# Kernel tuning notes

Measured on AMD Instinct MI355X. Metric: run time of the kernel, lower is better.

## Reference

```python
import jax, jax.numpy as jnp
import numpy as np
from jax import lax

EPS = 1e-5
HEADS = 4
NPOINT = 512


def _layernorm(x, g, b):
    mu = jnp.mean(x, axis=-1, keepdims=True)
    var = jnp.var(x, axis=-1, keepdims=True)
    return (x - mu) * lax.rsqrt(var + EPS) * g + b


def farthest_point_sample(xyz, npoint):
    # xyz: [B, N, 3] -> idx [B, npoint]  (canonical PointNet++ FPS, seeded at point 0)
    B, N, _ = xyz.shape

    def step(carry, _):
        dist, far = carry  # [B,N], [B]
        centroid = jnp.take_along_axis(xyz, far[:, None, None], axis=1)  # [B,1,3]
        d = jnp.sum((xyz - centroid) ** 2, axis=-1)  # [B,N]
        dist = jnp.minimum(dist, d)
        nxt = jnp.argmax(dist, axis=1).astype(jnp.int32)
        return (dist, nxt), far

    init = (jnp.full((B, N), 1e10, xyz.dtype), jnp.zeros((B,), jnp.int32))
    _, idx = lax.scan(step, init, None, length=npoint)  # [npoint, B]
    return idx.T  # [B, npoint]


def index_points(points, idx):
    # points: [B, N, D], idx: [B, S] -> [B, S, D]
    return jnp.take_along_axis(points, idx[..., None], axis=1)


def setup_inputs() -> dict:
    key = jax.random.key(0)
    ks = iter(jax.random.split(key, 16))
    B, N, Cin, D, Dff, Dout = 8, 2048, 64, 128, 512, 256
    w = lambda k, s: (jax.random.normal(k, s, jnp.float32) * 0.02)
    inp = {
        "xyz": jax.random.normal(next(ks), (B, 3, N), jnp.float32),
        "points": jax.random.normal(next(ks), (B, Cin, N), jnp.float32),
        "W_proj": w(next(ks), (D, Cin)), "b_proj": jnp.zeros((D,)),
        "bn1_g": jnp.ones((D,)), "bn1_b": jnp.zeros((D,)),
        "bn1_m": jnp.zeros((D,)), "bn1_v": jnp.ones((D,)),
        "W_pos": w(next(ks), (D, 3)), "b_pos": jnp.zeros((D,)),
        "Wq": w(next(ks), (D, D)), "bq": jnp.zeros((D,)),
        "Wk": w(next(ks), (D, D)), "bk": jnp.zeros((D,)),
        "Wv": w(next(ks), (D, D)), "bv": jnp.zeros((D,)),
        "Wo": w(next(ks), (D, D)), "bo": jnp.zeros((D,)),
        "ln1_g": jnp.ones((D,)), "ln1_b": jnp.zeros((D,)),
        "W1": w(next(ks), (Dff, D)), "b1": jnp.zeros((Dff,)),
        "W2": w(next(ks), (D, Dff)), "b2": jnp.zeros((D,)),
        "ln2_g": jnp.ones((D,)), "ln2_b": jnp.zeros((D,)),
        "W_fc": w(next(ks), (Dout, D + 3)), "b_fc": jnp.zeros((Dout,)),
        "bn2_g": jnp.ones((Dout,)), "bn2_b": jnp.zeros((Dout,)),
        "bn2_m": jnp.zeros((Dout,)), "bn2_v": jnp.ones((Dout,)),
    }
    return inp


def reference(xyz, points, W_proj, b_proj, bn1_g, bn1_b, bn1_m, bn1_v,
              W_pos, b_pos, Wq, bq, Wk, bk, Wv, bv, Wo, bo,
              ln1_g, ln1_b, W1, b1, W2, b2, ln2_g, ln2_b,
              W_fc, b_fc, bn2_g, bn2_b, bn2_m, bn2_v):
    B, _, N = xyz.shape
    D = W_proj.shape[0]
    hd = D // HEADS

    # project: pointwise conv + BN (inference), output [B, N, D]
    feat = jnp.einsum('dc,bcn->bnd', W_proj, points) + b_proj
    feat = (feat - bn1_m) * lax.rsqrt(bn1_v + EPS) * bn1_g + bn1_b

    # transformer block with xyz positional encoding
    pos = jnp.einsum('dc,bcn->bnd', W_pos, xyz) + b_pos
    x = feat + pos
    q = (x @ Wq.T + bq).reshape(B, N, HEADS, hd)
    k = (x @ Wk.T + bk).reshape(B, N, HEADS, hd)
    v = (x @ Wv.T + bv).reshape(B, N, HEADS, hd)
    scores = jnp.einsum('bnhd,bmhd->bhnm', q, k) / jnp.sqrt(jnp.float32(hd))
    attn = jax.nn.softmax(scores, axis=-1)
    o = jnp.einsum('bhnm,bmhd->bnhd', attn, v).reshape(B, N, D)
    x = _layernorm(x + (o @ Wo.T + bo), ln1_g, ln1_b)
    ffn = jax.nn.relu(x @ W1.T + b1) @ W2.T + b2
    features = _layernorm(x + ffn, ln2_g, ln2_b)  # [B, N, D]

    # sampling + gather
    xyz_t = jnp.transpose(xyz, (0, 2, 1))  # [B, N, 3]
    fps_idx = farthest_point_sample(xyz_t, NPOINT)  # [B, npoint]
    new_points = index_points(features, fps_idx)    # [B, npoint, D]
    new_xyz = index_points(xyz_t, fps_idx)          # [B, npoint, 3]

    cat = jnp.concatenate([new_points, new_xyz], axis=-1)  # [B, npoint, D+3]
    out = jnp.einsum('od,bnd->bon', W_fc, cat) + b_fc[None, :, None]
    out = (out - bn2_m[None, :, None]) * lax.rsqrt(bn2_v + EPS)[None, :, None] \
          * bn2_g[None, :, None] + bn2_b[None, :, None]
    out = jax.nn.relu(out)  # [B, Dout, npoint]

    return jnp.transpose(new_xyz, (0, 2, 1)), out
```

## Files before the change

### kernel.cpp

```cpp
#include <hip/hip_runtime.h>
#include <hip/hip_bf16.h>

#define B_    8
#define N_    2048
#define CIN_  64
#define D_    128
#define DFF_  512
#define DOUT_ 256
#define S_    512
#define H_    4
#define HD_   32
#define EPS_  1e-5f

typedef unsigned short u16;
typedef unsigned long long u64;
typedef __attribute__((ext_vector_type(8))) short short8v;
typedef __attribute__((ext_vector_type(4))) float f32x4;

__device__ __forceinline__ u16 f2bu(float f) {
  __hip_bfloat16 h = __float2bfloat16(f);
  return *(u16*)&h;
}
__device__ __forceinline__ float bu2f(u16 u) {
  __hip_bfloat16 h = *(__hip_bfloat16*)&u;
  return __bfloat162float(h);
}

#define OW_QKV 0
#define OW_O   49152
#define OW_1   65536
#define OW_2   131072
#define OW_FC  196608
#define OW_CAT 237568
#define NW_TOT 249856

__global__ __launch_bounds__(256) void prep_kernel(
    const float* __restrict__ Wq, const float* __restrict__ bq,
    const float* __restrict__ Wk, const float* __restrict__ bk,
    const float* __restrict__ Wv, const float* __restrict__ bv,
    const float* __restrict__ Wo, const float* __restrict__ W1,
    const float* __restrict__ W2, const float* __restrict__ Wfc,
    const float* __restrict__ bfc, const float* __restrict__ Wp,
    const float* __restrict__ bp, const float* __restrict__ Wpos,
    const float* __restrict__ bpos, const float* __restrict__ g1,
    const float* __restrict__ be1, const float* __restrict__ m1,
    const float* __restrict__ v1, const float* __restrict__ g2,
    const float* __restrict__ bb2, const float* __restrict__ m2,
    const float* __restrict__ v2, u16* __restrict__ wb,
    float* __restrict__ fb) {
  const float SC = 0.1767766952966369f;
  int i = blockIdx.x * 256 + threadIdx.x;
  if (i < OW_O) {
    int n = i >> 7, k = i & 127;
    float v = (n < 128) ? Wq[i] * SC
                        : (n < 256) ? Wk[(n - 128) * 128 + k]
                                    : Wv[(n - 256) * 128 + k];
    wb[OW_QKV + i] = f2bu(v);
  } else if (i < OW_1) {
    wb[i] = f2bu(Wo[i - OW_O]);
  } else if (i < OW_2) {
    wb[i] = f2bu(W1[i - OW_1]);
  } else if (i < OW_FC) {
    wb[i] = f2bu(W2[i - OW_2]);
  } else if (i < OW_CAT) {
    int j = i - OW_FC;
    int n = j / 160, c = j % 160;
    wb[i] = f2bu(c < 131 ? Wfc[n * 131 + c] : 0.f);
  } else if (i < NW_TOT) {
    int j = i - OW_CAT;
    int d = j / 96, c = j % 96;
    float v;
    if (c < 64) v = Wp[d * 64 + c] * (g1[d] * rsqrtf(v1[d] + EPS_));
    else if (c < 67) v = Wpos[d * 3 + (c - 64)];
    else v = 0.f;
    wb[i] = f2bu(v);
  } else if (i < NW_TOT + 384) {
    int n = i - NW_TOT;
    fb[n] = (n < 128) ? bq[n] * SC : (n < 256) ? bk[n - 128] : bv[n - 256];
  } else if (i < NW_TOT + 512) {
    int d = i - (NW_TOT + 384);
    float s1 = g1[d] * rsqrtf(v1[d] + EPS_);
    fb[384 + d] = (bp[d] - m1[d]) * s1 + be1[d] + bpos[d];
  } else if (i < NW_TOT + 768) {
    int n = i - (NW_TOT + 512);
    fb[512 + n] = g2[n] * rsqrtf(v2[n] + EPS_);
  } else if (i < NW_TOT + 1024) {
    int n = i - (NW_TOT + 768);
    float s = g2[n] * rsqrtf(v2[n] + EPS_);
    fb[768 + n] = bfc[n] * s + bb2[n] - m2[n] * s;
  }
}

#define FPS_SMEM 24704

template <int CTRL, int RM>
__device__ __forceinline__ float dppmax(float v) {
  int m = __builtin_amdgcn_update_dpp(__float_as_int(v), __float_as_int(v),
                                      CTRL, RM, 0xF, true);
  return fmaxf(v, __int_as_float(m));
}

__device__ __forceinline__ void fps_slice(
    char* smem, int b, const float* __restrict__ xyz,
    float* __restrict__ dist_ws, int* __restrict__ far_ws,
    int* __restrict__ idx_out, float* __restrict__ out0, int s0, int s1) {
  float* xs = (float*)smem;
  u64* keys = (u64*)(smem + 3 * N_ * 4);
  const int t = threadIdx.x, w = t >> 6, lane = t & 63;
  const float* xb = xyz + (size_t)b * 3 * N_;
  for (int i = t; i < 3 * N_; i += 256) xs[i] = xb[i];
  const int base = w * 512 + lane * 8;
  float* dw = dist_ws + b * N_;
  float dist[8];
  if (s0 == 0) {
#pragma unroll
    for (int j = 0; j < 8; j++) dist[j] = 1e10f;
  } else {
#pragma unroll
    for (int j = 0; j < 8; j++) dist[j] = dw[base + j];
  }
  int far = (s0 == 0) ? 0 : far_ws[b];
  __syncthreads();
  float px[8], py[8], pz[8];
#pragma unroll
  for (int j = 0; j < 8; j++) {
    px[j] = xs[base + j];
    py[j] = xs[N_ + base + j];
    pz[j] = xs[2 * N_ + base + j];
  }
  float cx = xs[far], cy = xs[N_ + far], cz = xs[2 * N_ + far];
  for (int s = s0; s < s1; s++) {
    if (t == 0) {
      idx_out[b * S_ + s] = far;
      out0[(size_t)b * 3 * S_ + s] = cx;
      out0[(size_t)b * 3 * S_ + S_ + s] = cy;
      out0[(size_t)b * 3 * S_ + 2 * S_ + s] = cz;
    }
    float best = -1.0f;
    int bestp = 0;
#pragma unroll
    for (int j = 0; j < 8; j++) {
      float dx = __fsub_rn(px[j], cx);
      float dy = __fsub_rn(py[j], cy);
      float dz = __fsub_rn(pz[j], cz);
      float d = __fadd_rn(__fadd_rn(__fmul_rn(dx, dx), __fmul_rn(dy, dy)),
                          __fmul_rn(dz, dz));
      float nd = fminf(dist[j], d);
      dist[j] = nd;
      if (nd > best) { best = nd; bestp = base + j; }
    }
    float m = best;
    m = dppmax<0x111, 0xF>(m);
    m = dppmax<0x112, 0xF>(m);
    m = dppmax<0x114, 0xF>(m);
    m = dppmax<0x118, 0xF>(m);
    m = dppmax<0x142, 0xA>(m);
    m = dppmax<0x143, 0xC>(m);
    float M = __int_as_float(__builtin_amdgcn_readlane(__float_as_int(m), 63));
    u64 mask = __ballot(best == M);
    int wl = __ffsll((long long)mask) - 1;
    int wp = __builtin_amdgcn_readlane(bestp, wl);
    if (lane == 0)
      keys[(s & 1) * 4 + w] = ((u64)__float_as_uint(M) << 32) |
                              (unsigned)(0xFFFFFFFFu - (unsigned)wp);
    __syncthreads();
    const u64* kp = keys + (s & 1) * 4;
    u64 k0 = kp[0], k1 = kp[1], k2 = kp[2], k3 = kp[3];
    u64 ka = k0 > k1 ? k0 : k1;
    u64 kb2 = k2 > k3 ? k2 : k3;
    u64 kk = ka > kb2 ? ka : kb2;
    far = (int)(0xFFFFFFFFu - (unsigned)kk);
    cx = xs[far];
    cy = xs[N_ + far];
    cz = xs[2 * N_ + far];
  }
#pragma unroll
  for (int j = 0; j < 8; j++) dw[base + j] = dist[j];
  if (t == 0) far_ws[b] = far;
}

template <int K, int KC, int ASTAGE, int EPI>
__global__ __launch_bounds__(256) void gemm_k(
    const u16* __restrict__ A, const u16* __restrict__ W,
    const float* __restrict__ srcf0, const float* __restrict__ srcf1,
    const int* __restrict__ fidx, const float* __restrict__ p0,
    const float* __restrict__ p1, const float* __restrict__ p2,
    const u16* __restrict__ resid, u16* __restrict__ outb,
    float* __restrict__ outf, int ntn, int fpsnb, int s0, int s1,
    const float* fxyz, float* fdist, int* ffar, int* fidxo, float* fout0) {
  constexpr int KP = KC + 8;
  constexpr int GEMM_SMEM = 2 * 128 * KP * 2;
  constexpr int SMEM = GEMM_SMEM > FPS_SMEM ? GEMM_SMEM : FPS_SMEM;
  __shared__ __align__(16) char smem[SMEM];
  if ((int)blockIdx.x < fpsnb) {
    fps_slice(smem, blockIdx.x, fxyz, fdist, ffar, fidxo, fout0, s0, s1);
    return;
  }
  u16 (*As)[KP] = (u16 (*)[KP])smem;
  u16 (*Ws)[KP] = (u16 (*)[KP])(smem + 128 * KP * 2);
  const int bid = blockIdx.x - fpsnb;
  const int mt = bid / ntn, nt = bid % ntn;
  const int t = threadIdx.x, w = t >> 6, lane = t & 63;
  const int g = lane >> 4, lr = lane & 15;

  f32x4 acc[2][8];
#pragma unroll
  for (int qf = 0; qf < 2; qf++)
#pragma unroll
    for (int nf = 0; nf < 8; nf++) acc[qf][nf] = {0.f, 0.f, 0.f, 0.f};

  for (int kc = 0; kc < K / KC; kc++) {
    __syncthreads();
    for (int i = t; i < 128 * (KC / 8); i += 256) {
      int row = i / (KC / 8), c8 = i % (KC / 8);
      *(short8v*)&Ws[row][c8 * 8] =
          *(const short8v*)(W + (size_t)(nt * 128 + row) * K + kc * KC + c8 * 8);
    }
    if constexpr (ASTAGE == 0) {
      for (int i = t; i < 128 * (KC / 8); i += 256) {
        int row = i / (KC / 8), c8 = i % (KC / 8);
        *(short8v*)&As[row][c8 * 8] =
            *(const short8v*)(A + (size_t)(mt * 128 + row) * K + kc * KC + c8 * 8);
      }
    } else if constexpr (ASTAGE == 1) {
      int bb = (mt * 128) >> 11, n0 = (mt * 128) & (N_ - 1);
      for (int i = t; i < 96 * 128; i += 256) {
        int c = i >> 7, n = i & 127;
        float v;
        if (c < 64) v = srcf0[((size_t)bb * CIN_ + c) * N_ + n0 + n];
        else if (c < 67) v = srcf1[((size_t)bb * 3 + (c - 64)) * N_ + n0 + n];
        else v = 0.f;
        As[n][c] = f2bu(v);
      }
    } else {
      int bb = (mt * 128) >> 9, sq0 = (mt * 128) & (S_ - 1);
      for (int i = t; i < 128 * 20; i += 256) {
        int row = i / 20, c8 = i % 20;
        int id = fidx[bb * S_ + sq0 + row];
        short8v val;
        if (c8 < 16) {
          val = *(const short8v*)(A + ((size_t)bb * N_ + id) * D_ + c8 * 8);
        } else if (c8 == 16) {
          val = short8v{0, 0, 0, 0, 0, 0, 0, 0};
          val[0] = (short)f2bu(srcf1[((size_t)bb * 3 + 0) * N_ + id]);
          val[1] = (short)f2bu(srcf1[((size_t)bb * 3 + 1) * N_ + id]);
          val[2] = (short)f2bu(srcf1[((size_t)bb * 3 + 2) * N_ + id]);
        } else {
          val = short8v{0, 0, 0, 0, 0, 0, 0, 0};
        }
        *(short8v*)&As[row][c8 * 8] = val;
      }
    }
    __syncthreads();
#pragma unroll
    for (int ks = 0; ks < KC / 32; ks++) {
      short8v a0 = *(const short8v*)&As[w * 32 + lr][ks * 32 + 8 * g];
      short8v a1 = *(const short8v*)&As[w * 32 + 16 + lr][ks * 32 + 8 * g];
#pragma unroll
      for (int nf = 0; nf < 8; nf++) {
        short8v bb = *(const short8v*)&Ws[nf * 16 + lr][ks * 32 + 8 * g];
        acc[0][nf] = __builtin_amdgcn_mfma_f32_16x16x32_bf16(a0, bb, acc[0][nf], 0, 0, 0);
        acc[1][nf] = __builtin_amdgcn_mfma_f32_16x16x32_bf16(a1, bb, acc[1][nf], 0, 0, 0);
      }
    }
  }

  if constexpr (EPI == 3) {
#pragma unroll
    for (int qf = 0; qf < 2; qf++) {
#pragma unroll
      for (int i = 0; i < 4; i++) {
        int m = mt * 128 + w * 32 + qf * 16 + 4 * g + i;
        float v[8], sm = 0.f, sq = 0.f;
#pragma unroll
        for (int nf = 0; nf < 8; nf++) {
          int n = nf * 16 + lr;
          float x = acc[qf][nf][i] + p0[n] + bu2f(resid[(size_t)m * D_ + n]);
          v[nf] = x;
          sm += x;
          sq += x * x;
        }
#pragma unroll
        for (int msk = 1; msk < 16; msk <<= 1) {
          sm += __shfl_xor(sm, msk);
          sq += __shfl_xor(sq, msk);
        }
        float mu = sm * (1.f / 128.f);
        float var = sq * (1.f / 128.f) - mu * mu;
        float rs = rsqrtf(var + EPS_);
#pragma unroll
        for (int nf = 0; nf < 8; nf++) {
          int n = nf * 16 + lr;
          outb[(size_t)m * D_ + n] = f2bu((v[nf] - mu) * rs * p1[n] + p2[n]);
        }
      }
    }
  } else {
#pragma unroll
    for (int qf = 0; qf < 2; qf++)
#pragma unroll
      for (int nf = 0; nf < 8; nf++)
#pragma unroll
        for (int i = 0; i < 4; i++) {
          int m = mt * 128 + w * 32 + qf * 16 + 4 * g + i;
          int nl = nf * 16 + lr;
          int n = nt * 128 + nl;
          float vv = acc[qf][nf][i];
          if constexpr (EPI == 0) {
            outb[(size_t)m * D_ + nl] = f2bu(vv + p0[n]);
          } else if constexpr (EPI == 1) {
            vv += p0[n];
            int which = n >> 7, h = (n >> 5) & 3, c = n & 31;
            int bb = m >> 11, tok = m & (N_ - 1);
            outb[(size_t)which * 2097152 +
                 (((size_t)bb * H_ + h) * N_ + tok) * HD_ + c] = f2bu(vv);
          } else if constexpr (EPI == 2) {
            outb[(size_t)m * DFF_ + n] = f2bu(fmaxf(vv + p0[n], 0.f));
          } else {
            float r = fmaxf(vv * p1[n] + p2[n], 0.f);
            outf[((size_t)(m >> 9) * DOUT_ + n) * S_ + (m & (S_ - 1))] = r;
          }
        }
  }
}

__global__ __launch_bounds__(256) void attn_mfma_kernel(
    const u16* __restrict__ qg, const u16* __restrict__ kg,
    const u16* __restrict__ vg, u16* __restrict__ o, int fpsnb, int s0, int s1,
    const float* fxyz, float* fdist, int* ffar, int* fidxo, float* fout0) {
  constexpr int ATTN_SMEM = 64 * 40 * 2 + 32 * 72 * 2 + 4 * 32 * 72 * 2;
  constexpr int SMEM = ATTN_SMEM > FPS_SMEM ? ATTN_SMEM : FPS_SMEM;
  __shared__ __align__(16) char smem[SMEM];
  if ((int)blockIdx.x < fpsnb) {
    fps_slice(smem, blockIdx.x, fxyz, fdist, ffar, fidxo, fout0, s0, s1);
    return;
  }
  u16 (*ks)[40] = (u16 (*)[40])smem;
  u16 (*vt)[72] = (u16 (*)[72])(smem + 5120);
  u16 (*ps)[32][72] = (u16 (*)[32][72])(smem + 5120 + 4608);

  const int bid = blockIdx.x - fpsnb;
  const int qt = bid & 15;
  const int bh = bid >> 4;
  const int b = bh >> 2, h = bh & 3;
  const int t = threadIdx.x;
  const int w = t >> 6, lane = t & 63, g = lane >> 4, lr = lane & 15;

  const int qbase = qt * 128 + w * 32;
  const u16* qrow = qg + ((size_t)bh * N_ + qbase) * HD_;
  short8v aq[2];
#pragma unroll
  for (int qf = 0; qf < 2; qf++)
    aq[qf] = *(const short8v*)(qrow + (qf * 16 + lr) * HD_ + 8 * g);

  const u16* kb = kg + (size_t)bh * N_ * HD_;
  const u16* vb = vg + (size_t)bh * N_ * HD_;

  const f32x4 fzero = {0.f, 0.f, 0.f, 0.f};
  float mrun[2][4], lrun[2][4];
  f32x4 acco[2][2];
#pragma unroll
  for (int qf = 0; qf < 2; qf++) {
#pragma unroll
    for (int i = 0; i < 4; i++) { mrun[qf][i] = -INFINITY; lrun[qf][i] = 0.f; }
    acco[qf][0] = fzero;
    acco[qf][1] = fzero;
  }

  const int srow = t >> 2, scol = (t & 3) * 8;

  for (int ch = 0; ch < 32; ch++) {
    __syncthreads();
    short8v kvv = *(const short8v*)(kb + (size_t)(ch * 64 + srow) * HD_ + scol);
    short8v vvv = *(const short8v*)(vb + (size_t)(ch * 64 + srow) * HD_ + scol);
    *(short8v*)(&ks[srow][scol]) = kvv;
#pragma unroll
    for (int e = 0; e < 8; e++) vt[scol + e][srow] = (u16)vvv[e];
    __syncthreads();

    f32x4 s[2][4];
#pragma unroll
    for (int qf = 0; qf < 2; qf++)
#pragma unroll
      for (int kt = 0; kt < 4; kt++) {
        short8v bk = *(const short8v*)(&ks[kt * 16 + lr][8 * g]);
        s[qf][kt] =
            __builtin_amdgcn_mfma_f32_16x16x32_bf16(aq[qf], bk, fzero, 0, 0, 0);
      }

#pragma unroll
    for (int qf = 0; qf < 2; qf++) {
#pragma unroll
      for (int i = 0; i < 4; i++) {
        float mx = fmaxf(fmaxf(s[qf][0][i], s[qf][1][i]),
                         fmaxf(s[qf][2][i], s[qf][3][i]));
#pragma unroll
        for (int m = 1; m < 16; m <<= 1) mx = fmaxf(mx, __shfl_xor(mx, m));
        float nm = fmaxf(mrun[qf][i], mx);
        float alpha = __expf(mrun[qf][i] - nm);
        mrun[qf][i] = nm;
        float psum = 0.f;
#pragma unroll
        for (int kt = 0; kt < 4; kt++) {
          float pv = __expf(s[qf][kt][i] - nm);
          psum += pv;
          ps[w][qf * 16 + 4 * g + i][kt * 16 + lr] = f2bu(pv);
        }
#pragma unroll
        for (int m = 1; m < 16; m <<= 1) psum += __shfl_xor(psum, m);
        lrun[qf][i] = lrun[qf][i] * alpha + psum;
        acco[qf][0][i] *= alpha;
        acco[qf][1][i] *= alpha;
      }
    }

#pragma unroll
    for (int qf = 0; qf < 2; qf++)
#pragma unroll
      for (int mc = 0; mc < 2; mc++) {
        short8v pa = *(const short8v*)(&ps[w][qf * 16 + lr][mc * 32 + 8 * g]);
#pragma unroll
        for (int dt = 0; dt < 2; dt++) {
          short8v bv = *(const short8v*)(&vt[dt * 16 + lr][mc * 32 + 8 * g]);
          acco[qf][dt] = __builtin_amdgcn_mfma_f32_16x16x32_bf16(
              pa, bv, acco[qf][dt], 0, 0, 0);
        }
      }
  }

#pragma unroll
  for (int qf = 0; qf < 2; qf++)
#pragma unroll
    for (int dt = 0; dt < 2; dt++)
#pragma unroll
      for (int i = 0; i < 4; i++) {
        int row = qbase + qf * 16 + 4 * g + i;
        o[((size_t)b * N_ + row) * D_ + h * HD_ + dt * 16 + lr] =
            f2bu(acco[qf][dt][i] / lrun[qf][i]);
      }
}

extern "C" void kernel_launch(void* const* d_in, const int* in_sizes, int n_in,
                              void* d_out, int out_size, void* d_ws, size_t ws_size,
                              hipStream_t stream) {
  const float* xyz    = (const float*)d_in[0];
  const float* points = (const float*)d_in[1];
  const float* Wp     = (const float*)d_in[2];
  const float* bp     = (const float*)d_in[3];
  const float* g1     = (const float*)d_in[4];
  const float* be1    = (const float*)d_in[5];
  const float* m1     = (const float*)d_in[6];
  const float* v1     = (const float*)d_in[7];
  const float* Wpos   = (const float*)d_in[8];
  const float* bpos   = (const float*)d_in[9];
  const float* Wq     = (const float*)d_in[10];
  const float* bq     = (const float*)d_in[11];
  const float* Wk     = (const float*)d_in[12];
  const float* bk     = (const float*)d_in[13];
  const float* Wv     = (const float*)d_in[14];
  const float* bv     = (const float*)d_in[15];
  const float* Wo     = (const float*)d_in[16];
  const float* bo     = (const float*)d_in[17];
  const float* lg1    = (const float*)d_in[18];
  const float* lb1    = (const float*)d_in[19];
  const float* W1     = (const float*)d_in[20];
  const float* b1     = (const float*)d_in[21];
  const float* W2     = (const float*)d_in[22];
  const float* b2p    = (const float*)d_in[23];
  const float* lg2    = (const float*)d_in[24];
  const float* lb2    = (const float*)d_in[25];
  const float* Wfc    = (const float*)d_in[26];
  const float* bfc    = (const float*)d_in[27];
  const float* g2     = (const float*)d_in[28];
  const float* bb2    = (const float*)d_in[29];
  const float* m2     = (const float*)d_in[30];
  const float* v2     = (const float*)d_in[31];

  float* out0 = (float*)d_out;
  float* out1 = out0 + (size_t)B_ * 3 * S_;

  char* ws = (char*)d_ws;
  int*   fps_idx = (int*)ws;
  u16*   wb      = (u16*)(ws + 16384);
  float* fb      = (float*)(ws + 516096);
  float* dist_ws = (float*)(ws + 520192);
  int*   far_ws  = (int*)(ws + 585728);
  const size_t MB = 1024 * 1024;
  u16* x     = (u16*)(ws + 1 * MB);
  u16* o     = (u16*)(ws + 5 * MB);
  u16* x2    = (u16*)(ws + 9 * MB);
  u16* feats = (u16*)(ws + 13 * MB);
  u16* qb    = (u16*)(ws + 17 * MB);
  u16* h     = (u16*)(ws + 29 * MB);

  prep_kernel<<<980, 256, 0, stream>>>(Wq, bq, Wk, bk, Wv, bv, Wo, W1, W2, Wfc,
                                       bfc, Wp, bp, Wpos, bpos, g1, be1, m1, v1,
                                       g2, bb2, m2, v2, wb, fb);

  gemm_k<96, 96, 1, 0><<<8 + 128, 256, 0, stream>>>(
      nullptr, wb + OW_CAT, points, xyz, nullptr, fb + 384, nullptr, nullptr,
      nullptr, x, nullptr, 1, 8, 0, 70, xyz, dist_ws, far_ws, fps_idx, out0);
  gemm_k<128, 128, 0, 1><<<8 + 384, 256, 0, stream>>>(
      x, wb + OW_QKV, nullptr, nullptr, nullptr, fb, nullptr, nullptr,
      nullptr, qb, nullptr, 3, 8, 70, 160, xyz, dist_ws, far_ws, fps_idx, out0);
  attn_mfma_kernel<<<8 + B_ * H_ * (N_ / 128), 256, 0, stream>>>(
      qb, qb + 2097152, qb + 2 * 2097152, o, 8, 160, 260, xyz, dist_ws, far_ws,
      fps_idx, out0);
  gemm_k<128, 128, 0, 3><<<8 + 128, 256, 0, stream>>>(
      o, wb + OW_O, nullptr, nullptr, nullptr, bo, lg1, lb1, x, x2, nullptr, 1,
      8, 260, 330, xyz, dist_ws, far_ws, fps_idx, out0);
  gemm_k<128, 128, 0, 2><<<8 + 512, 256, 0, stream>>>(
      x2, wb + OW_1, nullptr, nullptr, nullptr, b1, nullptr, nullptr,
      nullptr, h, nullptr, 4, 8, 330, 440, xyz, dist_ws, far_ws, fps_idx, out0);
  gemm_k<512, 128, 0, 3><<<8 + 128, 256, 0, stream>>>(
      h, wb + OW_2, nullptr, nullptr, nullptr, b2p, lg2, lb2, x2, feats,
      nullptr, 1, 8, 440, 512, xyz, dist_ws, far_ws, fps_idx, out0);
  gemm_k<160, 160, 2, 4><<<64, 256, 0, stream>>>(
      feats, wb + OW_FC, nullptr, xyz, fps_idx, nullptr, fb + 512, fb + 768,
      nullptr, nullptr, out1, 2, 0, 0, 0, nullptr, nullptr, nullptr, nullptr,
      nullptr);
}
```

Baseline: 367.2 us.

## Shrink FPS shared memory and restructure attention to transposed 16-row tiles

The FPS slice no longer stages all coordinates in shared memory. Each wave carries the winning point's coordinates through the reduction, writes them next to the key from the winning lane, and uses a raw barrier, which removes the coordinate reload after every step. The attention kernel now gives each wave 16 query rows instead of 32 and computes S^T with K as the A operand. This lets the softmax reductions use only two cross-lane shuffles and allows packed 64-bit stores, and it doubles the grid so more blocks co-reside, at the cost of reloading K/V tiles twice as often.

```diff
diff --git a/kernel.cpp b/kernel.cpp
--- a/kernel.cpp
+++ b/kernel.cpp
@@ -91,7 +91,7 @@
   }
 }
 
-#define FPS_SMEM 24704
+#define FPS_SMEM 256
 
 template <int CTRL, int RM>
 __device__ __forceinline__ float dppmax(float v) {
@@ -104,31 +104,26 @@
     char* smem, int b, const float* __restrict__ xyz,
     float* __restrict__ dist_ws, int* __restrict__ far_ws,
     int* __restrict__ idx_out, float* __restrict__ out0, int s0, int s1) {
-  float* xs = (float*)smem;
-  u64* keys = (u64*)(smem + 3 * N_ * 4);
+  u64* keys = (u64*)smem;
+  float* crd = (float*)(smem + 64);
   const int t = threadIdx.x, w = t >> 6, lane = t & 63;
   const float* xb = xyz + (size_t)b * 3 * N_;
-  for (int i = t; i < 3 * N_; i += 256) xs[i] = xb[i];
   const int base = w * 512 + lane * 8;
   float* dw = dist_ws + b * N_;
-  float dist[8];
-  if (s0 == 0) {
-#pragma unroll
-    for (int j = 0; j < 8; j++) dist[j] = 1e10f;
-  } else {
+  float px[8], py[8], pz[8], dist[8];
+#pragma unroll
+  for (int j = 0; j < 8; j++) {
+    px[j] = xb[base + j];
+    py[j] = xb[N_ + base + j];
+    pz[j] = xb[2 * N_ + base + j];
+    dist[j] = 1e10f;
+  }
+  if (s0 != 0) {
 #pragma unroll
     for (int j = 0; j < 8; j++) dist[j] = dw[base + j];
   }
   int far = (s0 == 0) ? 0 : far_ws[b];
-  __syncthreads();
-  float px[8], py[8], pz[8];
-#pragma unroll
-  for (int j = 0; j < 8; j++) {
-    px[j] = xs[base + j];
-    py[j] = xs[N_ + base + j];
-    pz[j] = xs[2 * N_ + base + j];
-  }
-  float cx = xs[far], cy = xs[N_ + far], cz = xs[2 * N_ + far];
+  float cx = xb[far], cy = xb[N_ + far], cz = xb[2 * N_ + far];
   for (int s = s0; s < s1; s++) {
     if (t == 0) {
       idx_out[b * S_ + s] = far;
@@ -136,7 +131,7 @@
       out0[(size_t)b * 3 * S_ + S_ + s] = cy;
       out0[(size_t)b * 3 * S_ + 2 * S_ + s] = cz;
     }
-    float best = -1.0f;
+    float best = -1.0f, bx = 0.f, by = 0.f, bz = 0.f;
     int bestp = 0;
 #pragma unroll
     for (int j = 0; j < 8; j++) {
@@ -147,7 +142,10 @@
                           __fmul_rn(dz, dz));
       float nd = fminf(dist[j], d);
       dist[j] = nd;
-      if (nd > best) { best = nd; bestp = base + j; }
+      if (nd > best) {
+        best = nd; bestp = base + j;
+        bx = px[j]; by = py[j]; bz = pz[j];
+      }
     }
     float m = best;
     m = dppmax<0x111, 0xF>(m);
@@ -159,20 +157,33 @@
     float M = __int_as_float(__builtin_amdgcn_readlane(__float_as_int(m), 63));
     u64 mask = __ballot(best == M);
     int wl = __ffsll((long long)mask) - 1;
-    int wp = __builtin_amdgcn_readlane(bestp, wl);
-    if (lane == 0)
-      keys[(s & 1) * 4 + w] = ((u64)__float_as_uint(M) << 32) |
-                              (unsigned)(0xFFFFFFFFu - (unsigned)wp);
-    __syncthreads();
-    const u64* kp = keys + (s & 1) * 4;
-    u64 k0 = kp[0], k1 = kp[1], k2 = kp[2], k3 = kp[3];
-    u64 ka = k0 > k1 ? k0 : k1;
-    u64 kb2 = k2 > k3 ? k2 : k3;
-    u64 kk = ka > kb2 ? ka : kb2;
+    if (lane == wl) {
+      int sb = (s & 1) * 4 + w;
+      keys[sb] = ((u64)__float_as_uint(M) << 32) |
+                 (unsigned)(0xFFFFFFFFu - (unsigned)bestp);
+      crd[sb * 3 + 0] = bx;
+      crd[sb * 3 + 1] = by;
+      crd[sb * 3 + 2] = bz;
+    }
+    asm volatile("s_waitcnt lgkmcnt(0)" ::: "memory");
+    __builtin_amdgcn_s_barrier();
+    asm volatile("" ::: "memory");
+    const int q0 = (s & 1) * 4;
+    u64 k0 = keys[q0], k1 = keys[q0 + 1], k2 = keys[q0 + 2], k3 = keys[q0 + 3];
+    float x0 = crd[q0 * 3 + 0], y0 = crd[q0 * 3 + 1], z0 = crd[q0 * 3 + 2];
+    float x1 = crd[q0 * 3 + 3], y1 = crd[q0 * 3 + 4], z1 = crd[q0 * 3 + 5];
+    float x2 = crd[q0 * 3 + 6], y2 = crd[q0 * 3 + 7], z2 = crd[q0 * 3 + 8];
+    float x3 = crd[q0 * 3 + 9], y3 = crd[q0 * 3 + 10], z3 = crd[q0 * 3 + 11];
+    bool c01 = k0 >= k1;
+    u64 ka = c01 ? k0 : k1;
+    float xa = c01 ? x0 : x1, ya = c01 ? y0 : y1, za = c01 ? z0 : z1;
+    bool c23 = k2 >= k3;
+    u64 kb = c23 ? k2 : k3;
+    float xv = c23 ? x2 : x3, yv = c23 ? y2 : y3, zv = c23 ? z2 : z3;
+    bool cf = ka >= kb;
+    u64 kk = cf ? ka : kb;
+    cx = cf ? xa : xv; cy = cf ? ya : yv; cz = cf ? za : zv;
     far = (int)(0xFFFFFFFFu - (unsigned)kk);
-    cx = xs[far];
-    cy = xs[N_ + far];
-    cz = xs[2 * N_ + far];
   }
 #pragma unroll
   for (int j = 0; j < 8; j++) dw[base + j] = dist[j];
@@ -328,44 +339,33 @@
     const u16* __restrict__ qg, const u16* __restrict__ kg,
     const u16* __restrict__ vg, u16* __restrict__ o, int fpsnb, int s0, int s1,
     const float* fxyz, float* fdist, int* ffar, int* fidxo, float* fout0) {
-  constexpr int ATTN_SMEM = 64 * 40 * 2 + 32 * 72 * 2 + 4 * 32 * 72 * 2;
+  constexpr int ATTN_SMEM = 64 * 40 * 2 + 32 * 72 * 2 + 4 * 16 * 72 * 2;
   constexpr int SMEM = ATTN_SMEM > FPS_SMEM ? ATTN_SMEM : FPS_SMEM;
   __shared__ __align__(16) char smem[SMEM];
   if ((int)blockIdx.x < fpsnb) {
     fps_slice(smem, blockIdx.x, fxyz, fdist, ffar, fidxo, fout0, s0, s1);
     return;
   }
+  const int t = threadIdx.x;
+  const int w = t >> 6, lane = t & 63, g = lane >> 4, lr = lane & 15;
   u16 (*ks)[40] = (u16 (*)[40])smem;
   u16 (*vt)[72] = (u16 (*)[72])(smem + 5120);
-  u16 (*ps)[32][72] = (u16 (*)[32][72])(smem + 5120 + 4608);
+  u16 (*psw)[72] = (u16 (*)[72])(smem + 9728) + w * 16;
 
   const int bid = blockIdx.x - fpsnb;
-  const int qt = bid & 15;
-  const int bh = bid >> 4;
+  const int qt = bid & 31;
+  const int bh = bid >> 5;
   const int b = bh >> 2, h = bh & 3;
-  const int t = threadIdx.x;
-  const int w = t >> 6, lane = t & 63, g = lane >> 4, lr = lane & 15;
-
-  const int qbase = qt * 128 + w * 32;
-  const u16* qrow = qg + ((size_t)bh * N_ + qbase) * HD_;
-  short8v aq[2];
-#pragma unroll
-  for (int qf = 0; qf < 2; qf++)
-    aq[qf] = *(const short8v*)(qrow + (qf * 16 + lr) * HD_ + 8 * g);
+  const int qrow = qt * 64 + w * 16 + lr;
+
+  short8v aq = *(const short8v*)(qg + ((size_t)bh * N_ + qrow) * HD_ + 8 * g);
 
   const u16* kb = kg + (size_t)bh * N_ * HD_;
   const u16* vb = vg + (size_t)bh * N_ * HD_;
 
   const f32x4 fzero = {0.f, 0.f, 0.f, 0.f};
-  float mrun[2][4], lrun[2][4];
-  f32x4 acco[2][2];
-#pragma unroll
-  for (int qf = 0; qf < 2; qf++) {
-#pragma unroll
-    for (int i = 0; i < 4; i++) { mrun[qf][i] = -INFINITY; lrun[qf][i] = 0.f; }
-    acco[qf][0] = fzero;
-    acco[qf][1] = fzero;
-  }
+  float mrun = -INFINITY, lrun = 0.f;
+  f32x4 acco[2] = {fzero, fzero};
 
   const int srow = t >> 2, scol = (t & 3) * 8;
 
@@ -378,66 +378,62 @@
     for (int e = 0; e < 8; e++) vt[scol + e][srow] = (u16)vvv[e];
     __syncthreads();
 
-    f32x4 s[2][4];
-#pragma unroll
-    for (int qf = 0; qf < 2; qf++)
-#pragma unroll
-      for (int kt = 0; kt < 4; kt++) {
-        short8v bk = *(const short8v*)(&ks[kt * 16 + lr][8 * g]);
-        s[qf][kt] =
-            __builtin_amdgcn_mfma_f32_16x16x32_bf16(aq[qf], bk, fzero, 0, 0, 0);
-      }
-
-#pragma unroll
-    for (int qf = 0; qf < 2; qf++) {
-#pragma unroll
-      for (int i = 0; i < 4; i++) {
-        float mx = fmaxf(fmaxf(s[qf][0][i], s[qf][1][i]),
-                         fmaxf(s[qf][2][i], s[qf][3][i]));
-#pragma unroll
-        for (int m = 1; m < 16; m <<= 1) mx = fmaxf(mx, __shfl_xor(mx, m));
-        float nm = fmaxf(mrun[qf][i], mx);
-        float alpha = __expf(mrun[qf][i] - nm);
-        mrun[qf][i] = nm;
-        float psum = 0.f;
-#pragma unroll
-        for (int kt = 0; kt < 4; kt++) {
-          float pv = __expf(s[qf][kt][i] - nm);
-          psum += pv;
-          ps[w][qf * 16 + 4 * g + i][kt * 16 + lr] = f2bu(pv);
-        }
-#pragma unroll
-        for (int m = 1; m < 16; m <<= 1) psum += __shfl_xor(psum, m);
-        lrun[qf][i] = lrun[qf][i] * alpha + psum;
-        acco[qf][0][i] *= alpha;
-        acco[qf][1][i] *= alpha;
-      }
-    }
-
-#pragma unroll
-    for (int qf = 0; qf < 2; qf++)
-#pragma unroll
-      for (int mc = 0; mc < 2; mc++) {
-        short8v pa = *(const short8v*)(&ps[w][qf * 16 + lr][mc * 32 + 8 * g]);
-#pragma unroll
-        for (int dt = 0; dt < 2; dt++) {
-          short8v bv = *(const short8v*)(&vt[dt * 16 + lr][mc * 32 + 8 * g]);
-          acco[qf][dt] = __builtin_amdgcn_mfma_f32_16x16x32_bf16(
-              pa, bv, acco[qf][dt], 0, 0, 0);
-        }
-      }
-  }
-
-#pragma unroll
-  for (int qf = 0; qf < 2; qf++)
+    f32x4 st[4];
+#pragma unroll
+    for (int kt = 0; kt < 4; kt++) {
+      short8v ak = *(const short8v*)(&ks[kt * 16 + lr][8 * g]);
+      st[kt] = __builtin_amdgcn_mfma_f32_16x16x32_bf16(ak, aq, fzero, 0, 0, 0);
+    }
+
+    float mx = -INFINITY;
+#pragma unroll
+    for (int kt = 0; kt < 4; kt++)
+#pragma unroll
+      for (int i = 0; i < 4; i++) mx = fmaxf(mx, st[kt][i]);
+    mx = fmaxf(mx, __shfl_xor(mx, 16));
+    mx = fmaxf(mx, __shfl_xor(mx, 32));
+    float nm = fmaxf(mrun, mx);
+    float alpha = __expf(mrun - nm);
+    mrun = nm;
+    float psum = 0.f;
+#pragma unroll
+    for (int kt = 0; kt < 4; kt++) {
+      float p0 = __expf(st[kt][0] - nm);
+      float p1 = __expf(st[kt][1] - nm);
+      float p2 = __expf(st[kt][2] - nm);
+      float p3 = __expf(st[kt][3] - nm);
+      psum += (p0 + p1) + (p2 + p3);
+      u64 pk = (u64)f2bu(p0) | ((u64)f2bu(p1) << 16) |
+               ((u64)f2bu(p2) << 32) | ((u64)f2bu(p3) << 48);
+      *(u64*)(&psw[lr][kt * 16 + 4 * g]) = pk;
+    }
+    psum += __shfl_xor(psum, 16);
+    psum += __shfl_xor(psum, 32);
+    lrun = lrun * alpha + psum;
 #pragma unroll
     for (int dt = 0; dt < 2; dt++)
 #pragma unroll
-      for (int i = 0; i < 4; i++) {
-        int row = qbase + qf * 16 + 4 * g + i;
-        o[((size_t)b * N_ + row) * D_ + h * HD_ + dt * 16 + lr] =
-            f2bu(acco[qf][dt][i] / lrun[qf][i]);
-      }
+      for (int i = 0; i < 4; i++) acco[dt][i] *= alpha;
+
+#pragma unroll
+    for (int mc = 0; mc < 2; mc++) {
+      short8v pb = *(const short8v*)(&psw[lr][mc * 32 + 8 * g]);
+#pragma unroll
+      for (int dt = 0; dt < 2; dt++) {
+        short8v av = *(const short8v*)(&vt[dt * 16 + lr][mc * 32 + 8 * g]);
+        acco[dt] = __builtin_amdgcn_mfma_f32_16x16x32_bf16(av, pb, acco[dt], 0, 0, 0);
+      }
+    }
+  }
+
+  float rl = 1.0f / lrun;
+#pragma unroll
+  for (int dt = 0; dt < 2; dt++) {
+    u64 pk = (u64)f2bu(acco[dt][0] * rl) | ((u64)f2bu(acco[dt][1] * rl) << 16) |
+             ((u64)f2bu(acco[dt][2] * rl) << 32) |
+             ((u64)f2bu(acco[dt][3] * rl) << 48);
+    *(u64*)(o + ((size_t)b * N_ + qrow) * D_ + h * HD_ + dt * 16 + 4 * g) = pk;
+  }
 }
 
 extern "C" void kernel_launch(void* const* d_in, const int* in_sizes, int n_in,
@@ -503,7 +499,7 @@
   gemm_k<128, 128, 0, 1><<<8 + 384, 256, 0, stream>>>(
       x, wb + OW_QKV, nullptr, nullptr, nullptr, fb, nullptr, nullptr,
       nullptr, qb, nullptr, 3, 8, 70, 160, xyz, dist_ws, far_ws, fps_idx, out0);
-  attn_mfma_kernel<<<8 + B_ * H_ * (N_ / 128), 256, 0, stream>>>(
+  attn_mfma_kernel<<<8 + B_ * H_ * (N_ / 64), 256, 0, stream>>>(
       qb, qb + 2097152, qb + 2 * 2097152, o, 8, 160, 260, xyz, dist_ws, far_ws,
       fps_idx, out0);
   gemm_k<128, 128, 0, 3><<<8 + 128, 256, 0, stream>>>(
```

Result: no change. 360.6 us (-1.8%).
